# Optimization experiments

Hardware: AMD Instinct MI355X
Metric: run time of the kernel (lower is better)

Reference implementation:

```python
import jax, jax.numpy as jnp
import numpy as np

B, NUM_GENES, F = 8, 20000, 128
N, E, H = 50000, 800000, 128


def setup_inputs() -> dict:
    key = jax.random.key(0)
    k = jax.random.split(key, 8)
    gene_emb = jax.random.normal(k[0], (B, NUM_GENES, F), dtype=jnp.float32)
    W1 = jax.random.normal(k[1], (F, H), dtype=jnp.float32) * 0.05
    b1 = jnp.zeros((H,), dtype=jnp.float32)
    W2 = jax.random.normal(k[2], (H, H), dtype=jnp.float32) * 0.05
    b2 = jnp.zeros((H,), dtype=jnp.float32)
    global_ids = jax.random.randint(k[3], (N,), 0, NUM_GENES, dtype=jnp.int64)
    edge_index = jax.random.randint(k[4], (2, E), 0, N, dtype=jnp.int64)
    return {"gene_emb": gene_emb, "W1": W1, "b1": b1, "W2": W2, "b2": b2,
            "global_ids": global_ids, "edge_index": edge_index}


def reference(gene_emb, W1, b1, W2, b2, global_ids, edge_index):
    n = global_ids.shape[0]
    # GCN normalization with self-loops (PyG GCNConv default):
    # A_hat = A + I, deg over target nodes, norm = d^{-1/2}[src] * d^{-1/2}[dst]
    loop = jnp.arange(n)
    src = jnp.concatenate([edge_index[0], loop])  # [E+N]
    dst = jnp.concatenate([edge_index[1], loop])  # [E+N]
    deg = jnp.zeros((n,), gene_emb.dtype).at[dst].add(1.0)
    dinv = jax.lax.rsqrt(deg)  # deg >= 1 thanks to self-loops
    norm = (dinv[src] * dinv[dst])[None, :, None]  # [1, E+N, 1]

    def gcn(x, W, b):
        h = x @ W                                   # [B, N, H] transform first (linear commutes)
        msg = h[:, src, :] * norm                   # gather + scale: [B, E+N, H]
        agg = jnp.zeros_like(h).at[:, dst].add(msg)  # scatter-add over targets
        return agg + b

    x = gene_emb[:, global_ids, :]                  # [B, N, F] node feature gather
    x = jax.nn.relu(gcn(x, W1, b1))
    x = gcn(x, W2, b2)
    # global_mean_pool: each batch replica is one whole graph -> mean over nodes
    return x.mean(axis=1)                           # [B, H]
```

## Files before the change

### kernel.cpp

```cpp
#include <hip/hip_runtime.h>

#define NG 20000
#define BB 8
#define FD 128

typedef unsigned int uint;
typedef unsigned short ushort;
typedef __attribute__((ext_vector_type(8))) short short8v;
typedef __attribute__((ext_vector_type(4))) float float4v;
typedef __attribute__((ext_vector_type(4))) int int4v;
typedef __attribute__((ext_vector_type(2))) float f2v;

__device__ f2v llvm_rbl_v2f32(int4v srsrc, int voffset, int soffset, int aux)
    __asm("llvm.amdgcn.raw.buffer.load.v2f32");

__device__ __forceinline__ int4v make_srsrc(const void* p) {
    int4v r;
    r.x = (int)(uint)(uintptr_t)p;
    r.y = (int)(uint)((uintptr_t)p >> 32);
    r.z = -1;
    r.w = 0x00020000;
    return r;
}

__device__ __forceinline__ ushort f2bf(float x) {
    uint u = __float_as_uint(x);
    u += 0x7FFFu + ((u >> 16) & 1u);
    return (ushort)(u >> 16);
}
__device__ __forceinline__ float bf_lo(uint u) { return __uint_as_float(u << 16); }
__device__ __forceinline__ float bf_hi(uint u) { return __uint_as_float(u & 0xFFFF0000u); }

__global__ void k_setup(int4* csrz, int zn4, float* deg, float* s_acc,
                        const float* __restrict__ W1, ushort* w1t, int N) {
    int i = blockIdx.x * blockDim.x + threadIdx.x;
    if (i < zn4) csrz[i] = make_int4(0, 0, 0, 0);
    if (i < N) deg[i] = 1.0f;
    if (i < BB * FD) s_acc[i] = 0.0f;
    if (i < FD * FD) {
        int j = i >> 7, k = i & 127;
        w1t[i] = f2bf(W1[k * 128 + j]);
    }
}

__global__ void k_count(const int* __restrict__ dst, float* deg, int E) {
    int e = blockIdx.x * blockDim.x + threadIdx.x;
    if (e < E) atomicAdd(&deg[dst[e]], 1.0f);
}

__global__ void k_scanA(const float* __restrict__ deg, float* dinv, float* cval,
                        float* wself, int* padcnt, int* offs, int* bsums, int N) {
    __shared__ int sd[256];
    int t = threadIdx.x, idx = blockIdx.x * 256 + t;
    int v = 0;
    if (idx < N) {
        float d = deg[idx];
        dinv[idx]  = rsqrtf(d);
        float iv = 1.0f / d;
        cval[idx]  = iv;
        wself[idx] = iv;
        v = ((int)d + 7) & ~7;
        padcnt[idx] = v;
    }
    sd[t] = v; __syncthreads();
    for (int o = 1; o < 256; o <<= 1) {
        int x = (t >= o) ? sd[t - o] : 0;
        __syncthreads();
        sd[t] += x;
        __syncthreads();
    }
    if (idx < N) offs[idx] = sd[t] - v;
    if (t == 255) bsums[blockIdx.x] = sd[255];
}

__global__ void k_scan2(int* bsums, int nb) {
    __shared__ int sd[256];
    int t = threadIdx.x;
    int v = (t < nb) ? bsums[t] : 0;
    sd[t] = v; __syncthreads();
    for (int o = 1; o < 256; o <<= 1) {
        int x = (t >= o) ? sd[t - o] : 0;
        __syncthreads();
        sd[t] += x;
        __syncthreads();
    }
    if (t < nb) bsums[t] = sd[t] - v;
}

__global__ void k_scanB(int* offs, const int* __restrict__ bsums,
                        const int* __restrict__ gid, const float* __restrict__ wself,
                        int* cursor, int2* csr, int N) {
    int i = blockIdx.x * blockDim.x + threadIdx.x;
    if (i < N) {
        int o = offs[i] + bsums[blockIdx.x];
        offs[i] = o;
        csr[o] = make_int2(gid[i], __float_as_int(wself[i]));
        cursor[i] = 1;
    }
}

__global__ void k_fill(const int* __restrict__ src, const int* __restrict__ dst,
                       const int* __restrict__ gid, const float* __restrict__ dinv,
                       float* cval, const int* __restrict__ offs, int* cursor,
                       int2* csr, int E) {
    int e = blockIdx.x * blockDim.x + threadIdx.x;
    if (e >= E) return;
    int s = src[e], d = dst[e];
    float nrm = dinv[s] * dinv[d];
    atomicAdd(&cval[s], nrm);
    int pos = atomicAdd(&cursor[d], 1);
    csr[offs[d] + pos] = make_int2(gid[s], __float_as_int(nrm));
}

__global__ __launch_bounds__(256, 3)
void k_h(const float* __restrict__ gene, const ushort* __restrict__ w1t,
         uint* __restrict__ h2u) {
    __shared__ __align__(16) char smem[49152];
    ushort* Al = (ushort*)smem;
    ushort* Bl = (ushort*)(smem + 16384);
    float*  Cl = (float*)smem;
    int t = threadIdx.x;
    int p    = blockIdx.x & 3;
    int tile = blockIdx.x >> 2;
    int g0   = tile * 32;

#pragma unroll
    for (int s = 0; s < 8; s++) {
        int f = t + s * 256;
        int r = f >> 5, k0 = (f & 31) * 4;
        int bb = 2 * p + (r >> 5);
        int gg = g0 + (r & 31);
        float4 v = *(const float4*)(gene + ((size_t)bb * NG + gg) * 128 + k0);
        ushort4 u;
        u.x = f2bf(v.x); u.y = f2bf(v.y); u.z = f2bf(v.z); u.w = f2bf(v.w);
        int byte = (r * 256 + k0 * 2) ^ ((r & 7) << 4);
        *(ushort4*)((char*)Al + byte) = u;
    }
#pragma unroll
    for (int s = 0; s < 8; s++) {
        int f = t + s * 256;
        int j = f >> 4, k0 = (f & 15) * 8;
        uint4 v = *(const uint4*)(w1t + j * 128 + k0);
        int byte = (j * 256 + k0 * 2) ^ ((j & 7) << 4);
        *(uint4*)((char*)Bl + byte) = v;
    }
    __syncthreads();

    int wid = t >> 6, lane = t & 63;
    int r0 = wid * 16;
    int lrow = lane & 15, lhi = lane >> 4;
    float4v acc[8];
#pragma unroll
    for (int nf = 0; nf < 8; nf++) acc[nf] = (float4v)(0.f);

#pragma unroll
    for (int c = 0; c < 4; c++) {
        int ra = r0 + lrow;
        int byteA = (ra * 256 + (c * 32 + lhi * 8) * 2) ^ ((ra & 7) << 4);
        short8v a = *(short8v*)((char*)Al + byteA);
#pragma unroll
        for (int nf = 0; nf < 8; nf++) {
            int jb = nf * 16 + lrow;
            int byteB = (jb * 256 + (c * 32 + lhi * 8) * 2) ^ ((jb & 7) << 4);
            short8v b = *(short8v*)((char*)Bl + byteB);
            acc[nf] = __builtin_amdgcn_mfma_f32_16x16x32_bf16(a, b, acc[nf], 0, 0, 0);
        }
    }
    __syncthreads();

#pragma unroll
    for (int nf = 0; nf < 8; nf++) {
#pragma unroll
        for (int q = 0; q < 4; q++) {
            Cl[(r0 + lhi * 4 + q) * 128 + nf * 16 + lrow] = acc[nf][q];
        }
    }
    __syncthreads();

#pragma unroll
    for (int s = 0; s < 16; s++) {
        int flat = t + s * 256;
        int gi = flat >> 7, cc = flat & 127;
        float lo = Cl[gi * 128 + cc];
        float hi = Cl[(32 + gi) * 128 + cc];
        uint u = (uint)f2bf(lo) | ((uint)f2bf(hi) << 16);
        h2u[((size_t)p * NG + g0 + gi) * 128 + cc] = u;
    }
}

__global__ __launch_bounds__(512)
void k_aggp(const uint* __restrict__ hp, const int2* __restrict__ csr,
            const int* __restrict__ offs, const int* __restrict__ padcnt,
            const float* __restrict__ cval, const float* __restrict__ b1,
            float* __restrict__ s_acc, int N, int npw) {
    int p    = blockIdx.x & 3;
    int wid  = threadIdx.x >> 6, lane = threadIdx.x & 63;
    int w    = __builtin_amdgcn_readfirstlane((blockIdx.x >> 2) * 8 + wid);
    int4v sr = make_srsrc(hp + (size_t)p * NG * 128);
    int voff = lane * 8;
    int l2 = lane * 2;
    float bx = b1[l2], by = b1[l2 + 1];
    float sx0 = 0.f, sx1 = 0.f, sy0 = 0.f, sy1 = 0.f;

    int i0 = w * npw;
    int i1 = min(N, i0 + npw);
    for (int i = i0; i < i1; ++i) {
        int   e  = offs[i];
        int   pc = padcnt[i];
        float cv = cval[i];
        float ax0 = 0.f, ax1 = 0.f, ay0 = 0.f, ay1 = 0.f;
        for (int q = 0; q < pc; q += 8) {
            int ee = e + q;
            int2 c0 = csr[ee],     c1 = csr[ee + 1], c2 = csr[ee + 2], c3 = csr[ee + 3];
            int2 c4 = csr[ee + 4], c5 = csr[ee + 5], c6 = csr[ee + 6], c7 = csr[ee + 7];
            f2v u0 = llvm_rbl_v2f32(sr, voff, c0.x << 9, 1);
            f2v u1 = llvm_rbl_v2f32(sr, voff, c1.x << 9, 1);
            f2v u2 = llvm_rbl_v2f32(sr, voff, c2.x << 9, 1);
            f2v u3 = llvm_rbl_v2f32(sr, voff, c3.x << 9, 1);
            f2v u4 = llvm_rbl_v2f32(sr, voff, c4.x << 9, 1);
            f2v u5 = llvm_rbl_v2f32(sr, voff, c5.x << 9, 1);
            f2v u6 = llvm_rbl_v2f32(sr, voff, c6.x << 9, 1);
            f2v u7 = llvm_rbl_v2f32(sr, voff, c7.x << 9, 1);
            float n0 = __int_as_float(c0.y), n1 = __int_as_float(c1.y);
            float n2 = __int_as_float(c2.y), n3 = __int_as_float(c3.y);
            float n4 = __int_as_float(c4.y), n5 = __int_as_float(c5.y);
            float n6 = __int_as_float(c6.y), n7 = __int_as_float(c7.y);
            uint a, b;
            a = __float_as_uint(u0.x); b = __float_as_uint(u0.y);
            ax0 = fmaf(n0, bf_lo(a), ax0); ax1 = fmaf(n0, bf_hi(a), ax1);
            ay0 = fmaf(n0, bf_lo(b), ay0); ay1 = fmaf(n0, bf_hi(b), ay1);
            a = __float_as_uint(u1.x); b = __float_as_uint(u1.y);
            ax0 = fmaf(n1, bf_lo(a), ax0); ax1 = fmaf(n1, bf_hi(a), ax1);
            ay0 = fmaf(n1, bf_lo(b), ay0); ay1 = fmaf(n1, bf_hi(b), ay1);
            a = __float_as_uint(u2.x); b = __float_as_uint(u2.y);
            ax0 = fmaf(n2, bf_lo(a), ax0); ax1 = fmaf(n2, bf_hi(a), ax1);
            ay0 = fmaf(n2, bf_lo(b), ay0); ay1 = fmaf(n2, bf_hi(b), ay1);
            a = __float_as_uint(u3.x); b = __float_as_uint(u3.y);
            ax0 = fmaf(n3, bf_lo(a), ax0); ax1 = fmaf(n3, bf_hi(a), ax1);
            ay0 = fmaf(n3, bf_lo(b), ay0); ay1 = fmaf(n3, bf_hi(b), ay1);
            a = __float_as_uint(u4.x); b = __float_as_uint(u4.y);
            ax0 = fmaf(n4, bf_lo(a), ax0); ax1 = fmaf(n4, bf_hi(a), ax1);
            ay0 = fmaf(n4, bf_lo(b), ay0); ay1 = fmaf(n4, bf_hi(b), ay1);
            a = __float_as_uint(u5.x); b = __float_as_uint(u5.y);
            ax0 = fmaf(n5, bf_lo(a), ax0); ax1 = fmaf(n5, bf_hi(a), ax1);
            ay0 = fmaf(n5, bf_lo(b), ay0); ay1 = fmaf(n5, bf_hi(b), ay1);
            a = __float_as_uint(u6.x); b = __float_as_uint(u6.y);
            ax0 = fmaf(n6, bf_lo(a), ax0); ax1 = fmaf(n6, bf_hi(a), ax1);
            ay0 = fmaf(n6, bf_lo(b), ay0); ay1 = fmaf(n6, bf_hi(b), ay1);
            a = __float_as_uint(u7.x); b = __float_as_uint(u7.y);
            ax0 = fmaf(n7, bf_lo(a), ax0); ax1 = fmaf(n7, bf_hi(a), ax1);
            ay0 = fmaf(n7, bf_lo(b), ay0); ay1 = fmaf(n7, bf_hi(b), ay1);
        }
        sx0 += cv * fmaxf(ax0 + bx, 0.f);
        sx1 += cv * fmaxf(ax1 + bx, 0.f);
        sy0 += cv * fmaxf(ay0 + by, 0.f);
        sy1 += cv * fmaxf(ay1 + by, 0.f);
    }

    __shared__ float red[8][256];
    red[wid][lane * 4 + 0] = sx0;
    red[wid][lane * 4 + 1] = sx1;
    red[wid][lane * 4 + 2] = sy0;
    red[wid][lane * 4 + 3] = sy1;
    __syncthreads();
    int t = threadIdx.x;
    if (t < 256) {
        float s = 0.f;
#pragma unroll
        for (int wv = 0; wv < 8; wv++) s += red[wv][t];
        int l = t >> 2, c = t & 3;
        atomicAdd(&s_acc[(2 * p + (c & 1)) * 128 + 2 * l + (c >> 1)], s);
    }
}

__global__ void k_final(const float* __restrict__ s_acc, const float* __restrict__ W2,
                        const float* __restrict__ b2, float* __restrict__ out, float invN) {
    __shared__ float ss[1024];
    int t = threadIdx.x;
    for (int idx = t; idx < 1024; idx += 128) ss[idx] = s_acc[idx];
    __syncthreads();
    float acc[8];
#pragma unroll
    for (int b = 0; b < 8; b++) acc[b] = 0.f;
    for (int k = 0; k < 128; k++) {
        float w = W2[k * 128 + t];
#pragma unroll
        for (int b = 0; b < 8; b++) acc[b] += ss[b * 128 + k] * w;
    }
    float bb = b2[t];
#pragma unroll
    for (int b = 0; b < 8; b++) out[b * 128 + t] = acc[b] * invN + bb;
}


extern "C" void kernel_launch(void* const* d_in, const int* in_sizes, int n_in,
                              void* d_out, int out_size, void* d_ws, size_t ws_size,
                              hipStream_t stream) {
    const float* gene = (const float*)d_in[0];
    const float* W1   = (const float*)d_in[1];
    const float* b1   = (const float*)d_in[2];
    const float* W2   = (const float*)d_in[3];
    const float* b2   = (const float*)d_in[4];
    const int*   gid  = (const int*)d_in[5];
    const int*   eidx = (const int*)d_in[6];
    int N = in_sizes[5];
    int E = in_sizes[6] / 2;
    const int* src = eidx;
    const int* dst = eidx + E;
    float* out = (float*)d_out;

    char* p = (char*)d_ws;
    auto alloc = [&](size_t bytes) -> char* {
        char* r = p; p += (bytes + 255) & ~(size_t)255; return r;
    };
    size_t csr_cap = (size_t)E + 8 * (size_t)N;
    float* deg    = (float*)alloc((size_t)N * 4);
    float* dinv   = (float*)alloc((size_t)N * 4);
    float* cval   = (float*)alloc((size_t)N * 4);
    float* wself  = (float*)alloc((size_t)N * 4);
    int*   padcnt = (int*)  alloc((size_t)N * 4);
    int*   offs   = (int*)  alloc((size_t)N * 4);
    int*   cursor = (int*)  alloc((size_t)N * 4);
    int*   bsums  = (int*)  alloc(256 * 4);
    int2*  csr    = (int2*) alloc(csr_cap * 8);
    float* s_acc  = (float*)alloc(1024 * 4);
    uint*  h2     = (uint*) alloc((size_t)NG * BB * FD * 2);
    ushort* w1t   = (ushort*)alloc(128 * 128 * 2);

    int nb = (N + 255) / 256;
    int eb = (E + 255) / 256;
    int zn4 = (int)(csr_cap * 8 / 16);
    int zb  = (zn4 + 255) / 256;

    const int NBLK = 2048;
    int wavesPerPair = (NBLK / 4) * 8;
    int npw = (N + wavesPerPair - 1) / wavesPerPair;

    k_setup<<<zb, 256, 0, stream>>>((int4*)csr, zn4, deg, s_acc, W1, w1t, N);
    k_count<<<eb, 256, 0, stream>>>(dst, deg, E);
    k_scanA<<<nb, 256, 0, stream>>>(deg, dinv, cval, wself, padcnt, offs, bsums, N);
    k_scan2<<<1, 256, 0, stream>>>(bsums, nb);
    k_scanB<<<nb, 256, 0, stream>>>(offs, bsums, gid, wself, cursor, csr, N);
    k_fill <<<eb, 256, 0, stream>>>(src, dst, gid, dinv, cval, offs, cursor, csr, E);
    k_h    <<<4 * (NG / 32), 256, 0, stream>>>(gene, w1t, h2);
    k_aggp <<<NBLK, 512, 0, stream>>>(h2, csr, offs, padcnt,
                                      cval, b1, s_acc, N, npw);
    k_final<<<1, 128, 0, stream>>>(s_acc, W2, b2, out, 1.0f / (float)N);
}
```

Baseline: 322.7 us.

## Fuse CSR fill with feature transform kernel, use integer degree atomics

Merges the edge-fill kernel and the gene-embedding GEMM into one launch, with the first blocks doing CSR fill and the rest computing h, so the two independent phases can overlap and one launch is saved. Degree counting switches from float atomics to integer atomics, with the self-loop added afterwards. The buffer-load cache-policy bit on the gather loads changes from 1 to 0. The fused kernel inherits the GEMM's 48KB shared memory and launch bounds for the fill blocks, which may lower occupancy for that part.

After: 306.6 us. -5.0%, faster.

```diff
diff --git a/kernel.cpp b/kernel.cpp
--- a/kernel.cpp
+++ b/kernel.cpp
@@ -31,11 +31,11 @@
 __device__ __forceinline__ float bf_lo(uint u) { return __uint_as_float(u << 16); }
 __device__ __forceinline__ float bf_hi(uint u) { return __uint_as_float(u & 0xFFFF0000u); }
 
-__global__ void k_setup(int4* csrz, int zn4, float* deg, float* s_acc,
+__global__ void k_setup(int4* csrz, int zn4, int* ideg, float* s_acc,
                         const float* __restrict__ W1, ushort* w1t, int N) {
     int i = blockIdx.x * blockDim.x + threadIdx.x;
     if (i < zn4) csrz[i] = make_int4(0, 0, 0, 0);
-    if (i < N) deg[i] = 1.0f;
+    if (i < N) ideg[i] = 0;
     if (i < BB * FD) s_acc[i] = 0.0f;
     if (i < FD * FD) {
         int j = i >> 7, k = i & 127;
@@ -43,23 +43,24 @@
     }
 }
 
-__global__ void k_count(const int* __restrict__ dst, float* deg, int E) {
+__global__ void k_count(const int* __restrict__ dst, int* ideg, int E) {
     int e = blockIdx.x * blockDim.x + threadIdx.x;
-    if (e < E) atomicAdd(&deg[dst[e]], 1.0f);
-}
-
-__global__ void k_scanA(const float* __restrict__ deg, float* dinv, float* cval,
+    if (e < E) atomicAdd(&ideg[dst[e]], 1);
+}
+
+__global__ void k_scanA(const int* __restrict__ ideg, float* dinv, float* cval,
                         float* wself, int* padcnt, int* offs, int* bsums, int N) {
     __shared__ int sd[256];
     int t = threadIdx.x, idx = blockIdx.x * 256 + t;
     int v = 0;
     if (idx < N) {
-        float d = deg[idx];
-        dinv[idx]  = rsqrtf(d);
-        float iv = 1.0f / d;
+        int d = ideg[idx] + 1;
+        float fd = (float)d;
+        dinv[idx]  = rsqrtf(fd);
+        float iv = 1.0f / fd;
         cval[idx]  = iv;
         wself[idx] = iv;
-        v = ((int)d + 7) & ~7;
+        v = (d + 7) & ~7;
         padcnt[idx] = v;
     }
     sd[t] = v; __syncthreads();
@@ -99,29 +100,31 @@
     }
 }
 
-__global__ void k_fill(const int* __restrict__ src, const int* __restrict__ dst,
-                       const int* __restrict__ gid, const float* __restrict__ dinv,
-                       float* cval, const int* __restrict__ offs, int* cursor,
-                       int2* csr, int E) {
-    int e = blockIdx.x * blockDim.x + threadIdx.x;
-    if (e >= E) return;
-    int s = src[e], d = dst[e];
-    float nrm = dinv[s] * dinv[d];
-    atomicAdd(&cval[s], nrm);
-    int pos = atomicAdd(&cursor[d], 1);
-    csr[offs[d] + pos] = make_int2(gid[s], __float_as_int(nrm));
-}
-
 __global__ __launch_bounds__(256, 3)
-void k_h(const float* __restrict__ gene, const ushort* __restrict__ w1t,
-         uint* __restrict__ h2u) {
+void k_fillh(const int* __restrict__ src, const int* __restrict__ dst,
+             const int* __restrict__ gid, const float* __restrict__ dinv,
+             float* cval, const int* __restrict__ offs, int* cursor,
+             int2* csr, int E, int eb,
+             const float* __restrict__ gene, const ushort* __restrict__ w1t,
+             uint* __restrict__ h2u) {
     __shared__ __align__(16) char smem[49152];
+    if ((int)blockIdx.x < eb) {
+        int e = blockIdx.x * 256 + threadIdx.x;
+        if (e >= E) return;
+        int s = src[e], d = dst[e];
+        float nrm = dinv[s] * dinv[d];
+        atomicAdd(&cval[s], nrm);
+        int pos = atomicAdd(&cursor[d], 1);
+        csr[offs[d] + pos] = make_int2(gid[s], __float_as_int(nrm));
+        return;
+    }
     ushort* Al = (ushort*)smem;
     ushort* Bl = (ushort*)(smem + 16384);
     float*  Cl = (float*)smem;
     int t = threadIdx.x;
-    int p    = blockIdx.x & 3;
-    int tile = blockIdx.x >> 2;
+    int hb   = blockIdx.x - eb;
+    int p    = hb & 3;
+    int tile = hb >> 2;
     int g0   = tile * 32;
 
 #pragma unroll
@@ -213,14 +216,14 @@
             int ee = e + q;
             int2 c0 = csr[ee],     c1 = csr[ee + 1], c2 = csr[ee + 2], c3 = csr[ee + 3];
             int2 c4 = csr[ee + 4], c5 = csr[ee + 5], c6 = csr[ee + 6], c7 = csr[ee + 7];
-            f2v u0 = llvm_rbl_v2f32(sr, voff, c0.x << 9, 1);
-            f2v u1 = llvm_rbl_v2f32(sr, voff, c1.x << 9, 1);
-            f2v u2 = llvm_rbl_v2f32(sr, voff, c2.x << 9, 1);
-            f2v u3 = llvm_rbl_v2f32(sr, voff, c3.x << 9, 1);
-            f2v u4 = llvm_rbl_v2f32(sr, voff, c4.x << 9, 1);
-            f2v u5 = llvm_rbl_v2f32(sr, voff, c5.x << 9, 1);
-            f2v u6 = llvm_rbl_v2f32(sr, voff, c6.x << 9, 1);
-            f2v u7 = llvm_rbl_v2f32(sr, voff, c7.x << 9, 1);
+            f2v u0 = llvm_rbl_v2f32(sr, voff, c0.x << 9, 0);
+            f2v u1 = llvm_rbl_v2f32(sr, voff, c1.x << 9, 0);
+            f2v u2 = llvm_rbl_v2f32(sr, voff, c2.x << 9, 0);
+            f2v u3 = llvm_rbl_v2f32(sr, voff, c3.x << 9, 0);
+            f2v u4 = llvm_rbl_v2f32(sr, voff, c4.x << 9, 0);
+            f2v u5 = llvm_rbl_v2f32(sr, voff, c5.x << 9, 0);
+            f2v u6 = llvm_rbl_v2f32(sr, voff, c6.x << 9, 0);
+            f2v u7 = llvm_rbl_v2f32(sr, voff, c7.x << 9, 0);
             float n0 = __int_as_float(c0.y), n1 = __int_as_float(c1.y);
             float n2 = __int_as_float(c2.y), n3 = __int_as_float(c3.y);
             float n4 = __int_as_float(c4.y), n5 = __int_as_float(c5.y);
@@ -314,7 +317,7 @@
         char* r = p; p += (bytes + 255) & ~(size_t)255; return r;
     };
     size_t csr_cap = (size_t)E + 8 * (size_t)N;
-    float* deg    = (float*)alloc((size_t)N * 4);
+    int*   ideg   = (int*)  alloc((size_t)N * 4);
     float* dinv   = (float*)alloc((size_t)N * 4);
     float* cval   = (float*)alloc((size_t)N * 4);
     float* wself  = (float*)alloc((size_t)N * 4);
@@ -331,18 +334,19 @@
     int eb = (E + 255) / 256;
     int zn4 = (int)(csr_cap * 8 / 16);
     int zb  = (zn4 + 255) / 256;
+    int hblk = 4 * (NG / 32);
 
     const int NBLK = 2048;
     int wavesPerPair = (NBLK / 4) * 8;
     int npw = (N + wavesPerPair - 1) / wavesPerPair;
 
-    k_setup<<<zb, 256, 0, stream>>>((int4*)csr, zn4, deg, s_acc, W1, w1t, N);
-    k_count<<<eb, 256, 0, stream>>>(dst, deg, E);
-    k_scanA<<<nb, 256, 0, stream>>>(deg, dinv, cval, wself, padcnt, offs, bsums, N);
+    k_setup<<<zb, 256, 0, stream>>>((int4*)csr, zn4, ideg, s_acc, W1, w1t, N);
+    k_count<<<eb, 256, 0, stream>>>(dst, ideg, E);
+    k_scanA<<<nb, 256, 0, stream>>>(ideg, dinv, cval, wself, padcnt, offs, bsums, N);
     k_scan2<<<1, 256, 0, stream>>>(bsums, nb);
     k_scanB<<<nb, 256, 0, stream>>>(offs, bsums, gid, wself, cursor, csr, N);
-    k_fill <<<eb, 256, 0, stream>>>(src, dst, gid, dinv, cval, offs, cursor, csr, E);
-    k_h    <<<4 * (NG / 32), 256, 0, stream>>>(gene, w1t, h2);
+    k_fillh<<<eb + hblk, 256, 0, stream>>>(src, dst, gid, dinv, cval, offs, cursor,
+                                           csr, E, eb, gene, w1t, h2);
     k_aggp <<<NBLK, 512, 0, stream>>>(h2, csr, offs, padcnt,
                                       cval, b1, s_acc, N, npw);
     k_final<<<1, 128, 0, stream>>>(s_acc, W2, b2, out, 1.0f / (float)N);
```
